# Kernel tuning notes

Measured on AMD Instinct MI355X. Metric: run time of the kernel, lower is better.

## Reference

```python
import jax, jax.numpy as jnp
from jax import lax
import numpy as np

STRIDE = 2
EXT_PAD = (2, 2)  # computed in __init__: (total_pad - inter_pad)//2 split symmetrically


def setup_inputs() -> dict:
    key = jax.random.key(0)
    k1, k2, k3 = jax.random.split(key, 3)
    x = jax.random.normal(k1, (32, 256, 32, 32), dtype=jnp.float32)
    # Conv kernel in OIHW layout: [out_chs, in_chs, kh, kw]
    W = jax.random.normal(k2, (128, 256, 4, 4), dtype=jnp.float32) * 0.05
    b = jax.random.normal(k3, (128,), dtype=jnp.float32) * 0.01
    return {"x": x, "W": W, "b": b}


def reference(x, W, b):
    # _Interpad: insert (stride-1) zeros between every pair of adjacent spatial
    # elements (not after the last one): new_size = (size-1)*stride + 1.
    B, C, H, Wd = x.shape
    s = STRIDE
    stuffed = jnp.zeros((B, C, (H - 1) * s + 1, (Wd - 1) * s + 1), dtype=x.dtype)
    stuffed = stuffed.at[:, :, ::s, ::s].set(x)
    # external zero padding
    p = EXT_PAD
    padded = jnp.pad(stuffed, ((0, 0), (0, 0), p, p))
    # standard (cross-correlation) conv, stride 1, dilation 1, valid padding
    y = lax.conv_general_dilated(
        padded, W,
        window_strides=(1, 1),
        padding='VALID',
        rhs_dilation=(1, 1),
        dimension_numbers=('NCHW', 'OIHW', 'NCHW'),
    )
    return y + b[None, :, None, None]
```

## Files before the change

kernel.cpp:

```cpp
#include <hip/hip_runtime.h>


typedef float  f32x4  __attribute__((ext_vector_type(4)));
typedef short  short8 __attribute__((ext_vector_type(8)));
typedef unsigned short ushort4v __attribute__((ext_vector_type(4)));
typedef unsigned short ushort8v __attribute__((ext_vector_type(8)));

__device__ __forceinline__ unsigned short f2bf(float f) {
    unsigned u = __builtin_bit_cast(unsigned, f);
    u += 0x7fffu + ((u >> 16) & 1u);
    return (unsigned short)(u >> 16);
}

__device__ __forceinline__ void ld_lds16(const unsigned short* g, unsigned short* l) {
    __builtin_amdgcn_global_load_lds(
        (const __attribute__((address_space(1))) unsigned int*)g,
        (__attribute__((address_space(3))) unsigned int*)l,
        16, 0, 0);
}

#define XP_U 288
#define XP_G 9792
#define XP_N 313344
#define WP_G 8192
#define WP_PI 262144

__global__ __launch_bounds__(256) void prepack_w2(const float* __restrict__ W,
                                                  unsigned short* __restrict__ wp) {
    int t = blockIdx.x * 256 + threadIdx.x;
    int o = t >> 8, c = t & 255;
    int g = c >> 3, c8 = c & 7;
    const float4* src = (const float4*)(W + (size_t)(o * 256 + c) * 16);
    float4 q0 = src[0], q1 = src[1], q2 = src[2], q3 = src[3];
    float rows[4][4] = {{q0.x,q0.y,q0.z,q0.w},{q1.x,q1.y,q1.z,q1.w},
                        {q2.x,q2.y,q2.z,q2.w},{q3.x,q3.y,q3.z,q3.w}};
    #pragma unroll
    for (int pi = 0; pi < 2; ++pi)
    #pragma unroll
    for (int pj = 0; pj < 2; ++pj)
    #pragma unroll
    for (int du = 0; du < 2; ++du)
    #pragma unroll
    for (int dv = 0; dv < 2; ++dv)
        wp[pi*WP_PI + g*WP_G + pj*4096 + (du*2+dv)*1024 + o*8 + c8] =
            f2bf(rows[pi+2*du][pj+2*dv]);
}

__global__ __launch_bounds__(256) void prepack_x(const float* __restrict__ x,
                                                 unsigned short* __restrict__ xp) {
    __shared__ unsigned short xt[256 * 32];
    const int tid = threadIdx.x;
    const int up  = blockIdx.x;
    const int n   = blockIdx.y;
    const bool interior = (up >= 1 && up <= 32);

    if (interior) {
        const int u = up - 1;
        #pragma unroll
        for (int k = 0; k < 8; ++k) {
            int idx4 = tid + k * 256;
            int c = idx4 >> 3, v4 = idx4 & 7;
            float4 val = *(const float4*)(x + ((size_t)(n*256 + c)*32 + u)*32 + v4*4);
            ushort4v s = { f2bf(val.x), f2bf(val.y), f2bf(val.z), f2bf(val.w) };
            *(ushort4v*)&xt[c*32 + v4*4] = s;
        }
        __syncthreads();
    }

    #pragma unroll
    for (int s = 0; s < 5; ++s) {
        int id = tid + s * 256;
        if (id < 1152) {
            int g = id / 36, vp = id % 36;
            ushort8v o8 = {0,0,0,0,0,0,0,0};
            if (interior && vp >= 1 && vp <= 32) {
                #pragma unroll
                for (int e = 0; e < 8; ++e)
                    o8[e] = xt[(g*8 + e)*32 + (vp - 1)];
            }
            *(ushort8v*)&xp[(size_t)n*XP_N + g*XP_G + up*XP_U + vp*8] = o8;
        }
    }
}

__global__ __launch_bounds__(256, 2) void tconv_main(
    const unsigned short* __restrict__ xp,
    const unsigned short* __restrict__ wp,
    const float* __restrict__ bias,
    float* __restrict__ out)
{
    __shared__ __align__(16) unsigned short lds[39552];
    unsigned short* xsh0 = lds;
    unsigned short* wsh0 = lds + 4 * 1440;

    const int tid  = threadIdx.x;
    const int lane = tid & 63;
    const int w    = tid >> 6;
    const int pjw  = w >> 1;
    const int half = w & 1;
    const int lg   = lane >> 4;
    const int ln   = lane & 15;
    const int du   = lg >> 1, dv = lg & 1;

    const int bid = blockIdx.x;
    const int wg  = (bid & 7) * 64 + (bid >> 3);
    const int n   = wg >> 4;
    const int aq  = (wg >> 1) & 7;
    const int pi  = wg & 1;
    const int a0  = aq * 4;

    const unsigned short* xpb = xp + (size_t)n * XP_N + (a0 + pi) * XP_U;
    const unsigned short* wpb = wp + pi * WP_PI;

    f32x4 acc[8][4];
    #pragma unroll
    for (int i = 0; i < 8; ++i)
        #pragma unroll
        for (int jj = 0; jj < 4; ++jj)
            acc[i][jj] = (f32x4){0.f, 0.f, 0.f, 0.f};

    auto stage = [&](int buf, int ch) {
        unsigned short* wd = wsh0 + buf * 8448;
        unsigned short* xd = xsh0 + buf * 1440;
        const unsigned short* ws = wpb + ch * WP_G;
        const unsigned short* xs = xpb + ch * XP_G;
        #pragma unroll
        for (int s = 0; s < 4; ++s) {
            int r = w * 2 + (s >> 1);
            int h = s & 1;
            ld_lds16(ws + r * 1024 + h * 512 + lane * 8,
                     wd + r * 1056 + h * 512);
        }
        if (lane < 36)
            ld_lds16(xs + w * XP_U + lane * 8, xd + w * 288);
        if (lane < 9)
            ld_lds16(xs + 4 * XP_U + (w * 9 + lane) * 8, xd + 4 * 288 + w * 72);
    };

    stage(0, 0);
    stage(1, 1);
    stage(2, 2);

    for (int ch = 0; ch < 32; ++ch) {
        const int cur = ch & 3;
        __builtin_amdgcn_sched_barrier(0);
        asm volatile("s_waitcnt vmcnt(12)" ::: "memory");
        __builtin_amdgcn_s_barrier();
        __builtin_amdgcn_sched_barrier(0);

        const unsigned short* xb = xsh0 + cur * 1440;
        const unsigned short* wb = wsh0 + cur * 8448;

        short8 bfr[4];
        #pragma unroll
        for (int jj = 0; jj < 4; ++jj) {
            int rr = half * 2 + (jj >> 1) + du;
            int vv = (jj & 1) * 16 + ln + pjw + dv;
            bfr[jj] = *(const short8*)&xb[(rr * 36 + vv) * 8];
        }

        const int chs = ch + 3;
        stage(chs & 3, chs & 31);

        #pragma unroll
        for (int i = 0; i < 8; ++i) {
            short8 av = *(const short8*)&wb[(pjw * 4 + lg) * 1056 + (i * 16 + ln) * 8];
            #pragma unroll
            for (int jj = 0; jj < 4; ++jj)
                acc[i][jj] = __builtin_amdgcn_mfma_f32_16x16x32_bf16(
                                 av, bfr[jj], acc[i][jj], 0, 0, 0);
        }
    }

    __syncthreads();

    float* epi = (float*)lds;
    #pragma unroll
    for (int i = 0; i < 8; ++i) {
        __syncthreads();
        f32x4 bv = *(const f32x4*)&bias[i * 16 + lg * 4];
        #pragma unroll
        for (int jj = 0; jj < 4; ++jj) {
            int ar = half * 2 + (jj >> 1);
            int b  = (jj & 1) * 16 + ln;
            #pragma unroll
            for (int r = 0; r < 4; ++r)
                epi[((lg * 4 + r) * 8 + ar * 2 + pjw) * 33 + b] = acc[i][jj][r] + bv[r];
        }
        __syncthreads();
        #pragma unroll
        for (int k = 0; k < 4; ++k) {
            int f   = tid + k * 256;
            int row = f >> 4;
            int q   = f & 15;
            float4 v;
            v.x = epi[(row * 2 + 0) * 33 + q * 2 + 0];
            v.y = epi[(row * 2 + 1) * 33 + q * 2 + 0];
            v.z = epi[(row * 2 + 0) * 33 + q * 2 + 1];
            v.w = epi[(row * 2 + 1) * 33 + q * 2 + 1];
            int o     = i * 16 + (row >> 2);
            int i_out = 2 * (a0 + (row & 3)) + pi;
            *(float4*)&out[(((size_t)n * 128 + o) * 64 + i_out) * 64 + q * 4] = v;
        }
    }
}

__global__ __launch_bounds__(256) void prepack_w(const float* __restrict__ W,
                                                 unsigned short* __restrict__ Wp) {
    int t = blockIdx.x * 256 + threadIdx.x;
    int o = t >> 8, c = t & 255;
    const float4* src = (const float4*)(W + (size_t)(o * 256 + c) * 16);
    float4 q0 = src[0], q1 = src[1], q2 = src[2], q3 = src[3];
    float rows[4][4] = {{q0.x,q0.y,q0.z,q0.w},{q1.x,q1.y,q1.z,q1.w},
                        {q2.x,q2.y,q2.z,q2.w},{q3.x,q3.y,q3.z,q3.w}};
    #pragma unroll
    for (int pi = 0; pi < 2; ++pi)
    #pragma unroll
    for (int pj = 0; pj < 2; ++pj)
    #pragma unroll
    for (int du = 0; du < 2; ++du)
    #pragma unroll
    for (int dv = 0; dv < 2; ++dv)
        Wp[((((pi*2+pj)*4 + du*2+dv)*128 + o)*256) + c] = f2bf(rows[pi+2*du][pj+2*dv]);
}

template<bool PRE>
__global__ __launch_bounds__(512, 2) void tconv_mfma(
    const float* __restrict__ x, const float* __restrict__ W,
    const unsigned short* __restrict__ Wp, const float* __restrict__ bias,
    float* __restrict__ out)
{
    __shared__ __align__(16) unsigned short xsh[2][9 * 34 * 8];
    __shared__ __align__(16) unsigned short wsh[2][2 * 4 * 128 * 8];

    const int tid = threadIdx.x;
    const int bid = blockIdx.x;
    const int pi  = bid & 1;
    const int aq  = (bid >> 1) & 3;
    const int n   = bid >> 3;
    const int a0  = aq * 8;
    const int u0  = a0 + pi - 1;

    const int l   = tid & 63;
    const int w   = tid >> 6;
    const int pjw = w >> 2;
    const int q   = w & 3;
    const int lg  = l >> 4;
    const int ln  = l & 15;

    const int sv = tid & 31;
    const int sg = tid >> 5;

    f32x4 acc[8][4];
    #pragma unroll
    for (int i = 0; i < 8; ++i)
        #pragma unroll
        for (int jj = 0; jj < 4; ++jj)
            acc[i][jj] = (f32x4){0.f, 0.f, 0.f, 0.f};

    float    xv[5];
    ushort4v wv[4];
    float4   wa[2], wb[2];

    auto stage_load = [&](int ch) {
        const int c0 = ch * 8;
        #pragma unroll
        for (int s = 0; s < 5; ++s) {
            int p = sg * 5 + s;
            if (p < 72) {
                int c = p & 7, rr = p >> 3;
                int u = u0 + rr;
                xv[s] = ((unsigned)u < 32u)
                      ? x[((n*256 + c0 + c)*32 + u)*32 + sv] : 0.f;
            }
        }
        if (PRE) {
            #pragma unroll
            for (int k = 0; k < 4; ++k) {
                int uu = tid + k * 512;
                int chalf = uu & 1, o = (uu >> 1) & 127;
                int sub = (uu >> 8) & 3, pjq = (uu >> 10) & 1;
                wv[k] = *(const ushort4v*)&Wp[(((pi*2 + pjq)*4 + sub)*128 + o)*256
                                              + c0 + chalf*4];
            }
        } else {
            #pragma unroll
            for (int k = 0; k < 2; ++k) {
                int pr = tid + k * 512;
                int o = pr >> 3, c = pr & 7;
                const float* base = W + ((o*256 + c0 + c) << 4) + pi*4;
                wa[k] = *(const float4*)base;
                wb[k] = *(const float4*)(base + 8);
            }
        }
    };

    auto stage_write = [&](int buf) {
        #pragma unroll
        for (int s = 0; s < 5; ++s) {
            int p = sg * 5 + s;
            if (p < 72) {
                int c = p & 7, rr = p >> 3;
                xsh[buf][(rr*34 + sv + 1)*8 + c] = f2bf(xv[s]);
            }
        }
        if (tid < 144) {
            int pr = tid >> 1;
            int rr = pr >> 3, c = pr & 7;
            int cw = (tid & 1) * 33;
            xsh[buf][(rr*34 + cw)*8 + c] = 0;
        }
        if (PRE) {
            #pragma unroll
            for (int k = 0; k < 4; ++k) {
                int uu = tid + k * 512;
                int chalf = uu & 1, o = (uu >> 1) & 127;
                int sub = (uu >> 8) & 3, pjq = (uu >> 10) & 1;
                *(ushort4v*)&wsh[buf][(((pjq*4 + sub)*128 + o)*8) + chalf*4] = wv[k];
            }
        } else {
            #pragma unroll
            for (int k = 0; k < 2; ++k) {
                int pr = tid + k * 512;
                int o = pr >> 3, c = pr & 7;
                float ra[4] = {wa[k].x, wa[k].y, wa[k].z, wa[k].w};
                float rb[4] = {wb[k].x, wb[k].y, wb[k].z, wb[k].w};
                #pragma unroll
                for (int pj2 = 0; pj2 < 2; ++pj2)
                #pragma unroll
                for (int duu = 0; duu < 2; ++duu)
                #pragma unroll
                for (int dvv = 0; dvv < 2; ++dvv) {
                    float val = duu ? rb[pj2 + 2*dvv] : ra[pj2 + 2*dvv];
                    wsh[buf][(((pj2*4 + duu*2 + dvv)*128 + o)*8) + c] = f2bf(val);
                }
            }
        }
    };

    stage_load(0);
    stage_write(0);
    __syncthreads();

    for (int ch = 0; ch < 32; ++ch) {
        const int cur = ch & 1;
        if (ch + 1 < 32) stage_load(ch + 1);

        short8 bfr[4];
        #pragma unroll
        for (int jj = 0; jj < 4; ++jj) {
            int arow = q*2 + (jj >> 1);
            int b    = (jj & 1)*16 + ln;
            int rr   = arow + (lg >> 1);
            int cw   = b + pjw + (lg & 1);
            bfr[jj]  = *(const short8*)&xsh[cur][(rr*34 + cw)*8];
        }
        #pragma unroll
        for (int i = 0; i < 8; ++i) {
            short8 av = *(const short8*)&wsh[cur][((pjw*4 + lg)*128 + i*16 + ln)*8];
            #pragma unroll
            for (int jj = 0; jj < 4; ++jj)
                acc[i][jj] = __builtin_amdgcn_mfma_f32_16x16x32_bf16(
                                 av, bfr[jj], acc[i][jj], 0, 0, 0);
        }

        if (ch + 1 < 32) stage_write(cur ^ 1);
        __syncthreads();
    }

    #pragma unroll
    for (int i = 0; i < 8; ++i) {
        const f32x4 bv = *(const f32x4*)&bias[i*16 + lg*4];
        #pragma unroll
        for (int jj = 0; jj < 4; ++jj) {
            int arow  = q*2 + (jj >> 1);
            int b     = (jj & 1)*16 + ln;
            int i_out = 2*(a0 + arow) + pi;
            int j_out = 2*b + pjw;
            int o0    = i*16 + lg*4;
            int base  = ((n*128 + o0)*64 + i_out)*64 + j_out;
            #pragma unroll
            for (int r = 0; r < 4; ++r)
                out[base + r*4096] = acc[i][jj][r] + bv[r];
        }
    }
}

extern "C" void kernel_launch(void* const* d_in, const int* in_sizes, int n_in,
                              void* d_out, int out_size, void* d_ws, size_t ws_size,
                              hipStream_t stream) {
    const float* x    = (const float*)d_in[0];
    const float* W    = (const float*)d_in[1];
    const float* bias = (const float*)d_in[2];
    float* out        = (float*)d_out;

    const size_t wp2_bytes = (size_t)2 * WP_PI * 2;
    const size_t xp_bytes  = (size_t)32 * XP_N * 2;
    if (ws_size >= wp2_bytes + xp_bytes) {
        unsigned short* wp2 = (unsigned short*)d_ws;
        unsigned short* xpp = (unsigned short*)((char*)d_ws + wp2_bytes);
        prepack_w2<<<128, 256, 0, stream>>>(W, wp2);
        prepack_x<<<dim3(34, 32), 256, 0, stream>>>(x, xpp);
        tconv_main<<<512, 256, 0, stream>>>(xpp, wp2, bias, out);
    } else if (ws_size >= (size_t)4*4*128*256*2) {
        unsigned short* Wp = (unsigned short*)d_ws;
        prepack_w<<<128, 256, 0, stream>>>(W, Wp);
        tconv_mfma<true><<<256, 512, 0, stream>>>(x, W, Wp, bias, out);
    } else {
        tconv_mfma<false><<<256, 512, 0, stream>>>(x, W, nullptr, bias, out);
    }
}
```

Measured before the change: 55.48 us.

## Load activation fragments directly from global into registers, keep LDS for weights

Stops staging the activation tile through LDS and instead loads each wave's B-fragments straight from global memory into double-buffered registers two chunks ahead. Only the weights remain in a 4-deep LDS ring, with the row pitch reduced from 1056 to 1040, and the vmcnt waits are reworked for the new load mix. The aim is to remove the LDS round trip and the ds_read traffic for activations and to shrink the LDS footprint. The cost is redundant, partly uncoalesced global loads for overlapping activation windows, plus higher register pressure from the two fragment buffers. The loop is also hand-unrolled by four with a separate tail.

```diff
diff --git a/kernel.cpp b/kernel.cpp
--- a/kernel.cpp
+++ b/kernel.cpp
@@ -24,6 +24,8 @@
 #define XP_N 313344
 #define WP_G 8192
 #define WP_PI 262144
+#define WROW 1040
+#define WBUFS 8320
 
 __global__ __launch_bounds__(256) void prepack_w2(const float* __restrict__ W,
                                                   unsigned short* __restrict__ wp) {
@@ -89,9 +91,8 @@
     const float* __restrict__ bias,
     float* __restrict__ out)
 {
-    __shared__ __align__(16) unsigned short lds[39552];
-    unsigned short* xsh0 = lds;
-    unsigned short* wsh0 = lds + 4 * 1440;
+    __shared__ __align__(16) unsigned short lds[33280];
+    unsigned short* wsh0 = lds;
 
     const int tid  = threadIdx.x;
     const int lane = tid & 63;
@@ -112,6 +113,15 @@
     const unsigned short* xpb = xp + (size_t)n * XP_N + (a0 + pi) * XP_U;
     const unsigned short* wpb = wp + pi * WP_PI;
 
+    int xoff[4];
+    #pragma unroll
+    for (int jj = 0; jj < 4; ++jj) {
+        int rr = half * 2 + (jj >> 1) + du;
+        int vv = (jj & 1) * 16 + ln + pjw + dv;
+        xoff[jj] = rr * XP_U + vv * 8;
+    }
+    const int wfoff = (pjw * 4 + lg) * WROW + ln * 8;
+
     f32x4 acc[8][4];
     #pragma unroll
     for (int i = 0; i < 8; ++i)
@@ -119,60 +129,66 @@
         for (int jj = 0; jj < 4; ++jj)
             acc[i][jj] = (f32x4){0.f, 0.f, 0.f, 0.f};
 
-    auto stage = [&](int buf, int ch) {
-        unsigned short* wd = wsh0 + buf * 8448;
-        unsigned short* xd = xsh0 + buf * 1440;
-        const unsigned short* ws = wpb + ch * WP_G;
-        const unsigned short* xs = xpb + ch * XP_G;
-        #pragma unroll
-        for (int s = 0; s < 4; ++s) {
-            int r = w * 2 + (s >> 1);
-            int h = s & 1;
-            ld_lds16(ws + r * 1024 + h * 512 + lane * 8,
-                     wd + r * 1056 + h * 512);
-        }
-        if (lane < 36)
-            ld_lds16(xs + w * XP_U + lane * 8, xd + w * 288);
-        if (lane < 9)
-            ld_lds16(xs + 4 * XP_U + (w * 9 + lane) * 8, xd + 4 * 288 + w * 72);
-    };
-
-    stage(0, 0);
-    stage(1, 1);
-    stage(2, 2);
-
-    for (int ch = 0; ch < 32; ++ch) {
-        const int cur = ch & 3;
-        __builtin_amdgcn_sched_barrier(0);
-        asm volatile("s_waitcnt vmcnt(12)" ::: "memory");
-        __builtin_amdgcn_s_barrier();
-        __builtin_amdgcn_sched_barrier(0);
-
-        const unsigned short* xb = xsh0 + cur * 1440;
-        const unsigned short* wb = wsh0 + cur * 8448;
-
-        short8 bfr[4];
-        #pragma unroll
-        for (int jj = 0; jj < 4; ++jj) {
-            int rr = half * 2 + (jj >> 1) + du;
-            int vv = (jj & 1) * 16 + ln + pjw + dv;
-            bfr[jj] = *(const short8*)&xb[(rr * 36 + vv) * 8];
-        }
-
-        const int chs = ch + 3;
-        stage(chs & 3, chs & 31);
-
-        #pragma unroll
-        for (int i = 0; i < 8; ++i) {
-            short8 av = *(const short8*)&wb[(pjw * 4 + lg) * 1056 + (i * 16 + ln) * 8];
-            #pragma unroll
-            for (int jj = 0; jj < 4; ++jj)
-                acc[i][jj] = __builtin_amdgcn_mfma_f32_16x16x32_bf16(
-                                 av, bfr[jj], acc[i][jj], 0, 0, 0);
-        }
-    }
-
-    __syncthreads();
+    short8 xA[4], xB[4];
+
+#define STAGE_W(CH, WBUF)                                                    \
+    { const unsigned short* ws_ = wpb + (size_t)(CH) * WP_G;                 \
+      unsigned short* wd_ = wsh0 + (WBUF) * WBUFS;                           \
+      _Pragma("unroll")                                                      \
+      for (int s_ = 0; s_ < 4; ++s_) {                                       \
+          int r_ = w * 2 + (s_ >> 1), h_ = s_ & 1;                           \
+          ld_lds16(ws_ + r_ * 1024 + h_ * 512 + lane * 8,                    \
+                   wd_ + r_ * WROW + h_ * 512); } }
+
+#define LOAD_X(CH, XS)                                                      \
+    { const unsigned short* xs_ = xpb + (size_t)(CH) * XP_G;                 \
+      _Pragma("unroll")                                                      \
+      for (int jj_ = 0; jj_ < 4; ++jj_)                                      \
+          XS[jj_] = *(const short8*)(xs_ + xoff[jj_]); }
+
+#define CHUNK(BUF, XS, CH, VMN, DO_W, DO_X)                                  \
+    {                                                                        \
+        __builtin_amdgcn_sched_barrier(0);                                   \
+        asm volatile("s_waitcnt vmcnt(" #VMN ")" ::: "memory");              \
+        __builtin_amdgcn_s_barrier();                                        \
+        __builtin_amdgcn_sched_barrier(0);                                   \
+        if (DO_W) STAGE_W((CH) + 3, ((BUF) + 3) & 3);                        \
+        const unsigned short* wb_ = wsh0 + (BUF) * WBUFS + wfoff;            \
+        _Pragma("unroll")                                                    \
+        for (int i_ = 0; i_ < 8; ++i_) {                                     \
+            short8 av_ = *(const short8*)&wb_[i_ * 128];                     \
+            _Pragma("unroll")                                                \
+            for (int jj_ = 0; jj_ < 4; ++jj_)                                \
+                acc[i_][jj_] = __builtin_amdgcn_mfma_f32_16x16x32_bf16(      \
+                    av_, XS[jj_], acc[i_][jj_], 0, 0, 0);                    \
+        }                                                                    \
+        if (DO_X) LOAD_X((CH) + 2, XS);                                      \
+    }
+
+    STAGE_W(0, 0);
+    STAGE_W(1, 1);
+    __builtin_amdgcn_sched_barrier(0);
+    LOAD_X(0, xA);
+    __builtin_amdgcn_sched_barrier(0);
+    STAGE_W(2, 2);
+    __builtin_amdgcn_sched_barrier(0);
+    LOAD_X(1, xB);
+    __builtin_amdgcn_sched_barrier(0);
+
+    for (int ch4 = 0; ch4 < 28; ch4 += 4) {
+        CHUNK(0, xA, ch4 + 0, 8, 1, 1);
+        CHUNK(1, xB, ch4 + 1, 8, 1, 1);
+        CHUNK(2, xA, ch4 + 2, 8, 1, 1);
+        CHUNK(3, xB, ch4 + 3, 8, 1, 1);
+    }
+    CHUNK(0, xA, 28, 8, 1, 1);
+    CHUNK(1, xB, 29, 8, 0, 1);
+    CHUNK(2, xA, 30, 4, 0, 0);
+    CHUNK(3, xB, 31, 0, 0, 0);
+
+#undef CHUNK
+#undef LOAD_X
+#undef STAGE_W
 
     float* epi = (float*)lds;
     #pragma unroll
```

After: 55.32 us. Within noise of the previous version (-0.3%).
